# Kernel tuning notes

Hardware: AMD Instinct MI355X
Metric: run time of the kernel (lower is better)

The kernel has to match this reference:

```python
import jax, jax.numpy as jnp
import numpy as np

HEADS = 12
HEAD_SIZE = 64
NEG_INF = -1000000000000.0


def setup_inputs() -> dict:
    key = jax.random.key(0)
    k1, k2 = jax.random.split(key)
    b, s, h = 8, 1024, 768
    inputs = jax.random.normal(k1, (b, s, h), dtype=jnp.float32)
    mask = jnp.ones((b, s), dtype=jnp.float32)
    W = jax.random.normal(k2, (h, HEADS * HEAD_SIZE * 2), dtype=jnp.float32) * 0.02
    bias = jnp.zeros((HEADS * HEAD_SIZE * 2,), dtype=jnp.float32)
    return {"inputs": inputs, "mask": mask, "W": W, "b": bias}


def _sinusoidal_pos(seq_len, dim, dtype):
    # bert4torch SinusoidalPositionEmbedding, mode 'zero': interleaved [sin, cos]
    pos = jnp.arange(seq_len, dtype=dtype)[:, None]              # [s,1]
    idx = jnp.arange(dim // 2, dtype=dtype)
    inv = jnp.power(jnp.asarray(10000.0, dtype), -2.0 * idx / dim)  # [d/2]
    ang = pos * inv[None, :]                                      # [s,d/2]
    return jnp.stack([jnp.sin(ang), jnp.cos(ang)], axis=-1).reshape(seq_len, dim)  # [s,d]


def reference(inputs, mask, W, b):
    bsz, s, _ = inputs.shape
    x = inputs @ W + b                                  # [b,s,heads*2*hs]
    x = x.reshape(bsz, s, HEADS, 2 * HEAD_SIZE)
    qw, kw = x[..., :HEAD_SIZE], x[..., HEAD_SIZE:]     # [b,s,h,d]

    pos = _sinusoidal_pos(s, HEAD_SIZE, x.dtype)        # [s,d]
    # NOTE: original torch code uses .repeat (tile), not repeat_interleave
    cos_pos = jnp.tile(pos[None, :, None, 1::2], (1, 1, 1, 2))  # [1,s,1,d]
    sin_pos = jnp.tile(pos[None, :, None, 0::2], (1, 1, 1, 2))

    def rotate(t):
        t2 = jnp.stack([-t[..., 1::2], t[..., 0::2]], axis=-1).reshape(t.shape)
        return t * cos_pos + t2 * sin_pos

    qw = rotate(qw)
    kw = rotate(kw)

    logits = jnp.einsum('bmhd,bnhd->bhmn', qw, kw)      # [b,h,s,s]

    m = mask.astype(logits.dtype)
    m_row = m[:, None, :, None]                          # axis = ndim-2
    m_col = m[:, None, None, :]                          # axis = ndim-1
    logits = logits * m_row + NEG_INF * (1.0 - m_row)
    logits = logits * m_col + NEG_INF * (1.0 - m_col)

    tril = jnp.tril(jnp.ones((s, s), dtype=logits.dtype), k=-1)
    logits = logits - tril * 1000000000000.0
    return logits / (HEAD_SIZE ** 0.5)
```

## Files before the change

kernel.cpp:

```cpp
#include <hip/hip_runtime.h>
#include <cstdint>
#include <cstddef>

#define HEADS 12
#define HD 64
#define BATCH 8
#define SEQ 1024
#define HIDDEN 768
#define NOUT (HEADS * HD * 2)
#define NEG -1000000000000.0f

using floatx4 = __attribute__((ext_vector_type(4))) float;
using shortx8 = __attribute__((ext_vector_type(8))) short;

static __device__ __forceinline__ unsigned short f2bf(float f) {
  union { float f; unsigned int u; } v; v.f = f;
  unsigned int u = v.u;
  u += 0x7fffu + ((u >> 16) & 1u);
  return (unsigned short)(u >> 16);
}

static __device__ __forceinline__ void async16(const void* g, void* l) {
  __builtin_amdgcn_global_load_lds(
      (const __attribute__((address_space(1))) unsigned int*)g,
      (__attribute__((address_space(3))) unsigned int*)l, 16, 0, 0);
}

__global__ void convert_inputs(const float* __restrict__ in,
                               unsigned short* __restrict__ out, int n4) {
  int i = blockIdx.x * blockDim.x + threadIdx.x;
  if (i < n4) {
    float4 f = ((const float4*)in)[i];
    ushort4 o;
    o.x = f2bf(f.x); o.y = f2bf(f.y); o.z = f2bf(f.z); o.w = f2bf(f.w);
    ((ushort4*)out)[i] = o;
  }
}

__global__ void transpose_w(const float* __restrict__ W,
                            unsigned short* __restrict__ Wt) {
  __shared__ float tile[32][33];
  int n0 = blockIdx.x * 32;
  int k0 = blockIdx.y * 32;
  for (int r = threadIdx.y; r < 32; r += 8)
    tile[r][threadIdx.x] = W[(size_t)(k0 + r) * NOUT + n0 + threadIdx.x];
  __syncthreads();
  for (int r = threadIdx.y; r < 32; r += 8)
    Wt[(size_t)(n0 + r) * HIDDEN + k0 + threadIdx.x] = f2bf(tile[threadIdx.x][r]);
}

__global__ void build_rope(float2* __restrict__ tab) {
  int idx = blockIdx.x * blockDim.x + threadIdx.x;
  int sp = idx >> 5, i = idx & 31;
  float inv = powf(10000.0f, -(float)i / 32.0f);
  float th = (float)sp * inv;
  float sn, cs;
  sincosf(th, &sn, &cs);
  tab[idx] = make_float2(cs, sn);
}

__global__ __launch_bounds__(256, 3) void gemm_rope(
    const unsigned short* __restrict__ A, const unsigned short* __restrict__ Bt,
    const float* __restrict__ bias, const float2* __restrict__ rope,
    unsigned short* __restrict__ qbuf, unsigned short* __restrict__ kbuf) {
  __shared__ unsigned short As[128 * 32];
  __shared__ unsigned short Bs[128 * 32];
  const int t = threadIdx.x;
  const int lane = t & 63, wave = t >> 6;
  const int wr = wave >> 1, wc = wave & 1;
  const int l15 = lane & 15, quad = lane >> 4;
  const int bn = blockIdx.x * 128;
  const int bm = blockIdx.y * 128;

  floatx4 acc[4][4] = {};
  const int s_row0 = t >> 2;
  const int s_pcb  = t & 3;

  for (int kt = 0; kt < HIDDEN; kt += 32) {
#pragma unroll
    for (int ch = 0; ch < 2; ch++) {
      int row = ch * 64 + s_row0;
      int cb  = s_pcb ^ ((row >> 1) & 3);
      async16(A  + (size_t)(bm + row) * HIDDEN + kt + cb * 8,
              (char*)As + ch * 4096 + t * 16);
      async16(Bt + (size_t)(bn + row) * HIDDEN + kt + cb * 8,
              (char*)Bs + ch * 4096 + t * 16);
    }
    __syncthreads();

    shortx8 af[4], bfr[4];
#pragma unroll
    for (int i = 0; i < 4; i++) {
      int rowA = wr * 64 + i * 16 + l15;
      int cbA  = quad ^ ((rowA >> 1) & 3);
      af[i] = *(const shortx8*)((const char*)As + rowA * 64 + cbA * 16);
      int rowB = wc * 64 + i * 16 + l15;
      int cbB  = quad ^ ((rowB >> 1) & 3);
      bfr[i] = *(const shortx8*)((const char*)Bs + rowB * 64 + cbB * 16);
    }
#pragma unroll
    for (int i = 0; i < 4; i++)
#pragma unroll
      for (int j = 0; j < 4; j++)
        acc[i][j] = __builtin_amdgcn_mfma_f32_16x16x32_bf16(af[i], bfr[j], acc[i][j], 0, 0, 0);
    __syncthreads();
  }

  const int mg_base = bm + wr * 64;
  const int ng_base = bn + wc * 64;
  const int h   = ng_base >> 7;
  const int isk = (ng_base >> 6) & 1;
  unsigned short* __restrict__ dst = isk ? kbuf : qbuf;
  const float sgn = (l15 & 1) ? 1.0f : -1.0f;
  float bia[4];
#pragma unroll
  for (int nt = 0; nt < 4; nt++) bia[nt] = bias[ng_base + nt * 16 + l15];

#pragma unroll
  for (int mt = 0; mt < 4; mt++) {
#pragma unroll
    for (int r = 0; r < 4; r++) {
      int m  = mg_base + mt * 16 + quad * 4 + r;
      int b  = m >> 10;
      int sp = m & 1023;
      float2 rc0 = rope[sp * 32 + l15];
      float2 rc1 = rope[sp * 32 + l15 + 16];
      size_t rowbase = ((size_t)(b * HEADS + h) * SEQ + sp) * HD;
#pragma unroll
      for (int nt = 0; nt < 4; nt++) {
        float v = acc[mt][nt][r] + bia[nt];
        float p = __shfl_xor(v, 1);
        float2 rc = (nt & 1) ? rc1 : rc0;
        float outv = v * rc.x + sgn * p * rc.y;
        float o2 = __shfl_xor(outv, 1);
        if (!(lane & 1)) {
          unsigned int pk = (unsigned int)f2bf(outv) | ((unsigned int)f2bf(o2) << 16);
          *(unsigned int*)(dst + rowbase + nt * 16 + l15) = pk;
        }
      }
    }
  }
}

__global__ __launch_bounds__(256, 4) void scores(
    const unsigned short* __restrict__ qbuf, const unsigned short* __restrict__ kbuf,
    const float* __restrict__ mask, float* __restrict__ out) {
  __shared__ unsigned short Qs[128 * 64];
  __shared__ unsigned short Ks[128 * 64];
  const int t = threadIdx.x;
  const int lane = t & 63, wave = t >> 6;
  const int wr = wave >> 1, wc = wave & 1;
  const int l15 = lane & 15, quad = lane >> 4;
  const int bh = blockIdx.z;
  const int b  = bh / HEADS;
  const int m0 = blockIdx.y * 128;
  const int n0 = blockIdx.x * 128;

  floatx4 acc[4][4] = {};

  const bool full_tril = (m0 >= n0 + 128);
  if (!full_tril) {
    const unsigned short* Qg = qbuf + (size_t)bh * SEQ * HD;
    const unsigned short* Kg = kbuf + (size_t)bh * SEQ * HD;
    const int s_row0 = t >> 3;
    const int s_pcb  = t & 7;
#pragma unroll
    for (int ch = 0; ch < 4; ch++) {
      int row = ch * 32 + s_row0;
      int cb  = s_pcb ^ (row & 7);
      async16(Qg + (size_t)(m0 + row) * HD + cb * 8, (char*)Qs + ch * 4096 + t * 16);
      async16(Kg + (size_t)(n0 + row) * HD + cb * 8, (char*)Ks + ch * 4096 + t * 16);
    }
    __syncthreads();

#pragma unroll
    for (int k0 = 0; k0 < 64; k0 += 32) {
      shortx8 af[4], bfr[4];
#pragma unroll
      for (int i = 0; i < 4; i++) {
        int rowA = wr * 64 + i * 16 + l15;
        int cbA  = (k0 / 8 + quad) ^ (rowA & 7);
        af[i] = *(const shortx8*)((const char*)Qs + rowA * 128 + cbA * 16);
        int rowB = wc * 64 + i * 16 + l15;
        int cbB  = (k0 / 8 + quad) ^ (rowB & 7);
        bfr[i] = *(const shortx8*)((const char*)Ks + rowB * 128 + cbB * 16);
      }
#pragma unroll
      for (int i = 0; i < 4; i++)
#pragma unroll
        for (int j = 0; j < 4; j++)
          acc[i][j] = __builtin_amdgcn_mfma_f32_16x16x32_bf16(af[i], bfr[j], acc[i][j], 0, 0, 0);
    }
  }

  const float* maskb = mask + (size_t)b * SEQ;
  float* outb = out + (size_t)bh * SEQ * SEQ;
  float mrowv[16], mcolv[4];
#pragma unroll
  for (int mt = 0; mt < 4; mt++)
#pragma unroll
    for (int r = 0; r < 4; r++)
      mrowv[mt * 4 + r] = maskb[m0 + wr * 64 + mt * 16 + quad * 4 + r];
#pragma unroll
  for (int nt = 0; nt < 4; nt++)
    mcolv[nt] = maskb[n0 + wc * 64 + nt * 16 + l15];

#pragma unroll
  for (int mt = 0; mt < 4; mt++) {
#pragma unroll
    for (int r = 0; r < 4; r++) {
      int m = m0 + wr * 64 + mt * 16 + quad * 4 + r;
      float mr = mrowv[mt * 4 + r];
      float off_r = NEG * (1.0f - mr);
#pragma unroll
      for (int nt = 0; nt < 4; nt++) {
        int n = n0 + wc * 64 + nt * 16 + l15;
        float mc = mcolv[nt];
        float v = fmaf(acc[mt][nt][r], mr, off_r);
        v = fmaf(v, mc, NEG * (1.0f - mc));
        if (m > n) v += NEG;
        outb[(size_t)m * SEQ + n] = v * 0.125f;
      }
    }
  }
}

extern "C" void kernel_launch(void* const* d_in, const int* in_sizes, int n_in,
                              void* d_out, int out_size, void* d_ws, size_t ws_size,
                              hipStream_t stream) {
  const float* inputs = (const float*)d_in[0];
  const float* mask   = (const float*)d_in[1];
  const float* W      = (const float*)d_in[2];
  const float* bias   = (const float*)d_in[3];
  float* out = (float*)d_out;

  char* ws = (char*)d_ws;
  const size_t A_BYTES  = (size_t)BATCH * SEQ * HIDDEN * 2;
  const size_t WT_BYTES = (size_t)NOUT * HIDDEN * 2;
  const size_t QK_BYTES = (size_t)BATCH * HEADS * SEQ * HD * 2;
  unsigned short* A_bf  = (unsigned short*)ws;
  unsigned short* Wt_bf = (unsigned short*)(ws + A_BYTES);
  unsigned short* qbuf  = (unsigned short*)(ws + A_BYTES + WT_BYTES);
  unsigned short* kbuf  = (unsigned short*)(ws + A_BYTES + WT_BYTES + QK_BYTES);
  float2* rope          = (float2*)(ws + A_BYTES + WT_BYTES + 2 * QK_BYTES);

  int n4 = BATCH * SEQ * HIDDEN / 4;
  convert_inputs<<<(n4 + 255) / 256, 256, 0, stream>>>(inputs, A_bf, n4);
  transpose_w<<<dim3(NOUT / 32, HIDDEN / 32), dim3(32, 8), 0, stream>>>(W, Wt_bf);
  build_rope<<<128, 256, 0, stream>>>(rope);
  gemm_rope<<<dim3(NOUT / 128, 8192 / 128), 256, 0, stream>>>(A_bf, Wt_bf, bias, rope, qbuf, kbuf);
  scores<<<dim3(SEQ / 128, SEQ / 128, BATCH * HEADS), 256, 0, stream>>>(qbuf, kbuf, mask, out);
}
```

Measured before the change: 478.9 us.

## Permute B/K tile rows so each lane owns four contiguous output columns

Loads of the weight and key tiles are remapped with an interleaving permutation, so each lane's MFMA accumulators cover four adjacent output columns. The projection epilogue can then apply bias and RoPE with float4 loads and no cross-lane shuffles, writing 8-byte stores. The scores epilogue writes float4 nontemporal stores and skips per-element tril comparisons for tiles entirely above or below the diagonal. This targets the store bandwidth of the large fp32 logits output, at the cost of more complex index mapping.

Result: faster. 455.6 us (-4.9%).

```diff
diff --git a/kernel.cpp b/kernel.cpp
--- a/kernel.cpp
+++ b/kernel.cpp
@@ -24,6 +24,10 @@
   __builtin_amdgcn_global_load_lds(
       (const __attribute__((address_space(1))) unsigned int*)g,
       (__attribute__((address_space(3))) unsigned int*)l, 16, 0, 0);
+}
+
+static __device__ __forceinline__ int interleave_g(int p) {
+  return (p & 0xC0) | ((p >> 4) & 3) | ((p & 15) << 2);
 }
 
 __global__ void convert_inputs(const float* __restrict__ in,
@@ -83,7 +87,7 @@
       int cb  = s_pcb ^ ((row >> 1) & 3);
       async16(A  + (size_t)(bm + row) * HIDDEN + kt + cb * 8,
               (char*)As + ch * 4096 + t * 16);
-      async16(Bt + (size_t)(bn + row) * HIDDEN + kt + cb * 8,
+      async16(Bt + (size_t)(bn + interleave_g(row)) * HIDDEN + kt + cb * 8,
               (char*)Bs + ch * 4096 + t * 16);
     }
     __syncthreads();
@@ -111,10 +115,9 @@
   const int h   = ng_base >> 7;
   const int isk = (ng_base >> 6) & 1;
   unsigned short* __restrict__ dst = isk ? kbuf : qbuf;
-  const float sgn = (l15 & 1) ? 1.0f : -1.0f;
-  float bia[4];
-#pragma unroll
-  for (int nt = 0; nt < 4; nt++) bia[nt] = bias[ng_base + nt * 16 + l15];
+  const int jb = 4 * l15;
+  const float4 bia = *(const float4*)(bias + ng_base + jb);
+  const int ri = 4 * (l15 & 7);
 
 #pragma unroll
   for (int mt = 0; mt < 4; mt++) {
@@ -123,21 +126,21 @@
       int m  = mg_base + mt * 16 + quad * 4 + r;
       int b  = m >> 10;
       int sp = m & 1023;
-      float2 rc0 = rope[sp * 32 + l15];
-      float2 rc1 = rope[sp * 32 + l15 + 16];
-      size_t rowbase = ((size_t)(b * HEADS + h) * SEQ + sp) * HD;
-#pragma unroll
-      for (int nt = 0; nt < 4; nt++) {
-        float v = acc[mt][nt][r] + bia[nt];
-        float p = __shfl_xor(v, 1);
-        float2 rc = (nt & 1) ? rc1 : rc0;
-        float outv = v * rc.x + sgn * p * rc.y;
-        float o2 = __shfl_xor(outv, 1);
-        if (!(lane & 1)) {
-          unsigned int pk = (unsigned int)f2bf(outv) | ((unsigned int)f2bf(o2) << 16);
-          *(unsigned int*)(dst + rowbase + nt * 16 + l15) = pk;
-        }
-      }
+      const float4* rs = (const float4*)(rope + sp * 32 + ri);
+      float4 r01 = rs[0];
+      float4 r23 = rs[1];
+      float v0 = acc[mt][0][r] + bia.x;
+      float v1 = acc[mt][1][r] + bia.y;
+      float v2 = acc[mt][2][r] + bia.z;
+      float v3 = acc[mt][3][r] + bia.w;
+      float o0 = v0 * r01.x - v1 * r01.y;
+      float o1 = v1 * r01.z + v0 * r01.w;
+      float o2 = v2 * r23.x - v3 * r23.y;
+      float o3 = v3 * r23.z + v2 * r23.w;
+      uint2 pk;
+      pk.x = (unsigned int)f2bf(o0) | ((unsigned int)f2bf(o1) << 16);
+      pk.y = (unsigned int)f2bf(o2) | ((unsigned int)f2bf(o3) << 16);
+      *(uint2*)(dst + ((size_t)(b * HEADS + h) * SEQ + sp) * HD + jb) = pk;
     }
   }
 }
@@ -158,8 +161,9 @@
 
   floatx4 acc[4][4] = {};
 
-  const bool full_tril = (m0 >= n0 + 128);
-  if (!full_tril) {
+  const int tril_mode = (m0 >= n0 + 128) ? 2 : ((m0 + 128 <= n0) ? 0 : 1);
+
+  if (tril_mode != 2) {
     const unsigned short* Qg = qbuf + (size_t)bh * SEQ * HD;
     const unsigned short* Kg = kbuf + (size_t)bh * SEQ * HD;
     const int s_row0 = t >> 3;
@@ -169,7 +173,8 @@
       int row = ch * 32 + s_row0;
       int cb  = s_pcb ^ (row & 7);
       async16(Qg + (size_t)(m0 + row) * HD + cb * 8, (char*)Qs + ch * 4096 + t * 16);
-      async16(Kg + (size_t)(n0 + row) * HD + cb * 8, (char*)Ks + ch * 4096 + t * 16);
+      async16(Kg + (size_t)(n0 + interleave_g(row)) * HD + cb * 8,
+              (char*)Ks + ch * 4096 + t * 16);
     }
     __syncthreads();
 
@@ -195,32 +200,29 @@
 
   const float* maskb = mask + (size_t)b * SEQ;
   float* outb = out + (size_t)bh * SEQ * SEQ;
-  float mrowv[16], mcolv[4];
-#pragma unroll
-  for (int mt = 0; mt < 4; mt++)
-#pragma unroll
-    for (int r = 0; r < 4; r++)
-      mrowv[mt * 4 + r] = maskb[m0 + wr * 64 + mt * 16 + quad * 4 + r];
-#pragma unroll
-  for (int nt = 0; nt < 4; nt++)
-    mcolv[nt] = maskb[n0 + wc * 64 + nt * 16 + l15];
+  const int nb = n0 + wc * 64 + 4 * l15;
+  const floatx4 mc4 = *(const floatx4*)(maskb + nb);
+  floatx4 offc;
+#pragma unroll
+  for (int c = 0; c < 4; c++) offc[c] = NEG * (1.0f - mc4[c]);
 
 #pragma unroll
   for (int mt = 0; mt < 4; mt++) {
 #pragma unroll
     for (int r = 0; r < 4; r++) {
       int m = m0 + wr * 64 + mt * 16 + quad * 4 + r;
-      float mr = mrowv[mt * 4 + r];
+      float mr = maskb[m];
       float off_r = NEG * (1.0f - mr);
-#pragma unroll
-      for (int nt = 0; nt < 4; nt++) {
-        int n = n0 + wc * 64 + nt * 16 + l15;
-        float mc = mcolv[nt];
-        float v = fmaf(acc[mt][nt][r], mr, off_r);
-        v = fmaf(v, mc, NEG * (1.0f - mc));
-        if (m > n) v += NEG;
-        outb[(size_t)m * SEQ + n] = v * 0.125f;
+      floatx4 v;
+#pragma unroll
+      for (int c = 0; c < 4; c++) {
+        float x = fmaf(acc[mt][c][r], mr, off_r);
+        x = fmaf(x, mc4[c], offc[c]);
+        if (tril_mode == 2) x += NEG;
+        else if (tril_mode == 1 && m > nb + c) x += NEG;
+        v[c] = x * 0.125f;
       }
+      __builtin_nontemporal_store(v, (floatx4*)(outb + (size_t)m * SEQ + nb));
     }
   }
 }
```
